# Kernel tuning notes

Measured on AMD Instinct MI355X. Metric: run time of the kernel, lower is better.

Reference implementation:

```python
import jax, jax.numpy as jnp
import numpy as np

# Model dims (ViT-Base @ 384)
L, H, D, HD, M, P, IMG, B, NC, CH = 12, 12, 768, 64, 3072, 16, 384, 32, 1000, 3
NPATCH = (IMG // P) ** 2  # 576
SCALE = 1.0 / np.sqrt(HD)


def setup_inputs() -> dict:
    key = jax.random.key(0)
    ks = iter(jax.random.split(key, 16))
    def n(shape, s=0.02):
        return (jax.random.normal(next(ks), shape, jnp.float32) * s).astype(jnp.float32)
    return dict(
        x=jax.random.normal(next(ks), (B, CH, IMG, IMG), jnp.float32),
        conv_w=n((D, CH, P, P)), conv_b=jnp.zeros((D,), jnp.float32),
        cls_token=jnp.zeros((1, 1, D), jnp.float32),
        pos_emb=n((1, NPATCH + 1, D), 1.0),
        ln1_g=jnp.ones((L, D), jnp.float32), ln1_b=jnp.zeros((L, D), jnp.float32),
        wqkv=n((L, H, D, 3 * HD)), bqkv=jnp.zeros((L, H, 3 * HD), jnp.float32),
        wmsa=n((L, D, D)), bmsa=jnp.zeros((L, D), jnp.float32),
        ln2_g=jnp.ones((L, D), jnp.float32), ln2_b=jnp.zeros((L, D), jnp.float32),
        lnm_g=jnp.ones((L, D), jnp.float32), lnm_b=jnp.zeros((L, D), jnp.float32),
        w1=n((L, D, M)), b1=jnp.zeros((L, M), jnp.float32),
        w2=n((L, M, D)), b2=jnp.zeros((L, D), jnp.float32),
        lnf_g=jnp.ones((D,), jnp.float32), lnf_b=jnp.zeros((D,), jnp.float32),
        whead=n((D, NC)), bhead=jnp.zeros((NC,), jnp.float32),
    )


def _ln(x, g, b, eps=1e-5):
    mu = jnp.mean(x, axis=-1, keepdims=True)
    var = jnp.mean(jnp.square(x - mu), axis=-1, keepdims=True)
    return (x - mu) * jax.lax.rsqrt(var + eps) * g + b


def _encoder_block(x, p):
    (ln1_g, ln1_b, wqkv, bqkv, wmsa, bmsa,
     ln2_g, ln2_b, lnm_g, lnm_b, w1, b1, w2, b2) = p
    b = x.shape[0]
    h = _ln(x, ln1_g, ln1_b)
    # batched per-head QKV (math identical to looping over H small Linears)
    qkv = jnp.einsum('bsd,hde->bhse', h, wqkv) + bqkv[:, None, :]  # [B,H,S,3*HD]
    q, k, v = jnp.split(qkv, 3, axis=-1)
    attn = jax.nn.softmax(jnp.einsum('bhqe,bhke->bhqk', q, k) * SCALE, axis=-1)
    o = jnp.einsum('bhqk,bhke->bhqe', attn, v)          # [B,H,S,HD]
    o = o.transpose(0, 2, 1, 3).reshape(b, -1, D)        # concat heads along feature
    msa = jnp.einsum('bsd,de->bse', o, wmsa) + bmsa
    x1 = h + msa                                          # residual around MSA (post-LN1)
    h2 = _ln(x1, ln2_g, ln2_b)
    h2 = _ln(h2, lnm_g, lnm_b)                            # MLPBlock's own LayerNorm (double LN, faithful)
    mlp = jnp.einsum('bsm,md->bsd', jax.nn.gelu(jnp.einsum('bsd,dm->bsm', h2, w1) + b1, approximate=False), w2) + b2
    return x1 + mlp, None


def reference(x, conv_w, conv_b, cls_token, pos_emb,
              ln1_g, ln1_b, wqkv, bqkv, wmsa, bmsa,
              ln2_g, ln2_b, lnm_g, lnm_b, w1, b1, w2, b2,
              lnf_g, lnf_b, whead, bhead):
    b = x.shape[0]
    # patchify conv (image divisible by patch, so F.pad is a no-op)
    t = jax.lax.conv_general_dilated(x, conv_w, (P, P), 'VALID',
                                     dimension_numbers=('NCHW', 'OIHW', 'NCHW'))
    t = t + conv_b[None, :, None, None]
    # faithful to torch .view(b, -1, embed_dim) on NCHW layout (channel-major flatten)
    t = t.reshape(b, -1, D)
    n = t.shape[1]
    t = jnp.concatenate([jnp.broadcast_to(cls_token, (b, 1, D)), t], axis=1)
    t = t + pos_emb[:, :n + 1]
    stacked = (ln1_g, ln1_b, wqkv, bqkv, wmsa, bmsa,
               ln2_g, ln2_b, lnm_g, lnm_b, w1, b1, w2, b2)
    t, _ = jax.lax.scan(_encoder_block, t, stacked)
    y = _ln(t[:, 0], lnf_g, lnf_b)
    y = jax.nn.softmax(jnp.einsum('bd,dc->bc', y, whead) + bhead, axis=-1)
    return y
```

## Files before the change

### kernel.cpp

```cpp
#include <hip/hip_runtime.h>

using f16   = _Float16;
using f16x8 = __attribute__((ext_vector_type(8))) _Float16;
using f32x4 = __attribute__((ext_vector_type(4))) float;

#define MPAD  18560
#define MREAL 18464
#define MCONV 18432
#define SEQ   577
#define SPAD  640
#define NHEAD 12
#define NBATCH 32
#define SCALE_ 0.125f

__device__ __forceinline__ void load_lds16(const void* g, void* l) {
  __builtin_amdgcn_global_load_lds(
      (const __attribute__((address_space(1))) void*)g,
      (__attribute__((address_space(3))) void*)l, 16, 0, 0);
}

template<int K, int EPI>
__global__ __launch_bounds__(256) void gemm_k(
    const f16* __restrict__ A, const f16* __restrict__ Bt,
    const float* __restrict__ bias, const float* __restrict__ res,
    float* __restrict__ o32, f16* __restrict__ o16a, f16* __restrict__ o16b,
    f16* __restrict__ o16c, const float* __restrict__ pos,
    const float* __restrict__ lng, const float* __restrict__ lnb,
    const float* __restrict__ stats, int N, int Mreal)
{
  static_assert(K % 64 == 0, "BK=64");
  __shared__ __align__(16) f16 As[128 * 64];
  __shared__ __align__(16) f16 Bs[128 * 64];
  const int tid = threadIdx.x;
  const int lane = tid & 63, wv = tid >> 6;

  const int gx = gridDim.x, gy = gridDim.y;
  const int nwg = gx * gy;
  const int flat = blockIdx.y * gx + blockIdx.x;
  const int xcd = flat & 7;
  const int qq = nwg >> 3, rr = nwg & 7;
  const int p_ = ((xcd < rr) ? xcd * (qq + 1) : rr * (qq + 1) + (xcd - rr) * qq)
                 + (flat >> 3);
  const int bandsz = gy * 6;
  const int band = p_ / bandsz, within = p_ - band * bandsz;
  const int byi = within / 6;
  const int bxi = band * 6 + (within - byi * 6);
  const int bm = byi << 7, bn = bxi << 7;

  const int wm = (wv >> 1) << 6, wn = (wv & 1) << 6;
  const int r16 = lane & 15, g4 = lane >> 4;
  const f32x4 Z4 = {0.f, 0.f, 0.f, 0.f};

  f32x4 acc[4][4];
#pragma unroll
  for (int m = 0; m < 4; ++m)
#pragma unroll
    for (int n = 0; n < 4; ++n) acc[m][n] = Z4;

  const int srow = lane >> 3;
  const int sgc  = (lane & 7) ^ srow;
  const f16* Agp = A  + (size_t)(bm + srow) * K + sgc * 8;
  const f16* Bgp = Bt + (size_t)(bn + srow) * K + sgc * 8;

  for (int k0 = 0; k0 < K; k0 += 64) {
#pragma unroll
    for (int j = 0; j < 4; ++j) {
      const size_t roff = (size_t)((wv * 4 + j) * 8) * K + k0;
      load_lds16(Agp + roff, As + (wv * 4 + j) * 512);
      load_lds16(Bgp + roff, Bs + (wv * 4 + j) * 512);
    }
    __syncthreads();
#pragma unroll
    for (int ks = 0; ks < 2; ++ks) {
      f16x8 af[4], bf[4];
#pragma unroll
      for (int m = 0; m < 4; ++m) {
        int row = wm + m * 16 + r16;
        af[m] = *(const f16x8*)(As + row * 64 + ((((ks << 2) | g4) ^ (row & 7)) << 3));
      }
#pragma unroll
      for (int n = 0; n < 4; ++n) {
        int row = wn + n * 16 + r16;
        bf[n] = *(const f16x8*)(Bs + row * 64 + ((((ks << 2) | g4) ^ (row & 7)) << 3));
      }
#pragma unroll
      for (int m = 0; m < 4; ++m)
#pragma unroll
        for (int n = 0; n < 4; ++n)
          acc[m][n] = __builtin_amdgcn_mfma_f32_16x16x32_f16(af[m], bf[n], acc[m][n], 0, 0, 0);
    }
    __syncthreads();
  }

#pragma unroll
  for (int m = 0; m < 4; ++m) {
#pragma unroll
    for (int n = 0; n < 4; ++n) {
#pragma unroll
      for (int r = 0; r < 4; ++r) {
        int grow = bm + wm + m * 16 + g4 * 4 + r;
        int gcol = bn + wn + n * 16 + r16;
        float v = acc[m][n][r];
        if constexpr (EPI == 0) {
          if (grow < Mreal) {
            int b = grow / 576, p = grow - b * 576;
            int i = gcol * 576 + p;
            int sp = i / 768, dd = i - sp * 768;
            o32[((size_t)(b * SEQ + sp + 1)) * 768 + dd] =
                v + bias[gcol] + pos[(size_t)(sp + 1) * 768 + dd];
          }
        } else if constexpr (EPI == 1) {
          if (grow < Mreal) {
            int b = grow / SEQ, s = grow - b * SEQ;
            int hq = gcol / 192, rem = gcol - hq * 192;
            int sel = rem >> 6, e = rem & 63;
            float val = v + bias[gcol];
            int bh = b * NHEAD + hq;
            if (sel == 0)      o16a[((size_t)bh * SPAD + s) * 64 + e] = (f16)val;
            else if (sel == 1) o16b[((size_t)bh * SPAD + s) * 64 + e] = (f16)val;
            else               o16c[((size_t)bh * 64 + e) * SPAD + s] = (f16)val;
          }
        } else if constexpr (EPI == 2) {
          size_t idx = (size_t)grow * N + gcol;
          o32[idx] = v + bias[gcol] + res[idx];
        } else if constexpr (EPI == 4) {
          if (grow < Mreal) {
            size_t idx = (size_t)grow * N + gcol;
            float mu = stats[2 * grow], rs = stats[2 * grow + 1];
            float h = (res[idx] - mu) * rs * lng[gcol] + lnb[gcol];
            o32[idx] = v + bias[gcol] + h;
          }
        } else {
          float val = v + bias[gcol];
          float gl = 0.5f * val * (1.0f + erff(val * 0.70710678f));
          o16a[(size_t)grow * N + gcol] = (f16)gl;
        }
      }
    }
  }
}

__device__ __forceinline__ void block_red2(float& a, float& b, float* sm, int tid) {
  __syncthreads();
#pragma unroll
  for (int d = 32; d; d >>= 1) { a += __shfl_down(a, d); b += __shfl_down(b, d); }
  if ((tid & 63) == 0) { int w = tid >> 6; sm[w] = a; sm[w + 4] = b; }
  __syncthreads();
  a = sm[0] + sm[1] + sm[2] + sm[3];
  b = sm[4] + sm[5] + sm[6] + sm[7];
}

__global__ __launch_bounds__(256) void ln_fwd(const float* __restrict__ X,
    const float* __restrict__ g, const float* __restrict__ bb,
    float* __restrict__ stats, f16* __restrict__ hh)
{
  int row = blockIdx.x, tid = threadIdx.x;
  const float* x = X + (size_t)row * 768;
  float v0 = x[tid], v1 = x[tid + 256], v2 = x[tid + 512];
  float s = v0 + v1 + v2, s2 = v0*v0 + v1*v1 + v2*v2;
  __shared__ float sm[8];
  block_red2(s, s2, sm, tid);
  float mu = s * (1.f/768.f);
  float var = s2 * (1.f/768.f) - mu * mu;
  float rs = rsqrtf(var + 1e-5f);
  if (tid == 0) { stats[2 * row] = mu; stats[2 * row + 1] = rs; }
  size_t base = (size_t)row * 768;
  hh[base + tid      ] = (f16)((v0 - mu) * rs * g[tid      ] + bb[tid      ]);
  hh[base + tid + 256] = (f16)((v1 - mu) * rs * g[tid + 256] + bb[tid + 256]);
  hh[base + tid + 512] = (f16)((v2 - mu) * rs * g[tid + 512] + bb[tid + 512]);
}

__global__ __launch_bounds__(256) void ln2_fwd(const float* __restrict__ X,
    const float* __restrict__ g2, const float* __restrict__ bb2,
    const float* __restrict__ gm, const float* __restrict__ bbm,
    f16* __restrict__ hh)
{
  int row = blockIdx.x, tid = threadIdx.x;
  const float* x = X + (size_t)row * 768;
  float v0 = x[tid], v1 = x[tid + 256], v2 = x[tid + 512];
  float s = v0 + v1 + v2, s2 = v0*v0 + v1*v1 + v2*v2;
  __shared__ float sm[8];
  block_red2(s, s2, sm, tid);
  float mu = s * (1.f/768.f), var = s2 * (1.f/768.f) - mu * mu;
  float rs = rsqrtf(var + 1e-5f);
  float y0 = (v0 - mu) * rs * g2[tid      ] + bb2[tid      ];
  float y1 = (v1 - mu) * rs * g2[tid + 256] + bb2[tid + 256];
  float y2 = (v2 - mu) * rs * g2[tid + 512] + bb2[tid + 512];
  s = y0 + y1 + y2; s2 = y0*y0 + y1*y1 + y2*y2;
  block_red2(s, s2, sm, tid);
  mu = s * (1.f/768.f); var = s2 * (1.f/768.f) - mu * mu;
  rs = rsqrtf(var + 1e-5f);
  size_t base = (size_t)row * 768;
  hh[base + tid      ] = (f16)((y0 - mu) * rs * gm[tid      ] + bbm[tid      ]);
  hh[base + tid + 256] = (f16)((y1 - mu) * rs * gm[tid + 256] + bbm[tid + 256]);
  hh[base + tid + 512] = (f16)((y2 - mu) * rs * gm[tid + 512] + bbm[tid + 512]);
}

__global__ __launch_bounds__(256) void attn_k(const f16* __restrict__ qbuf,
    const f16* __restrict__ kbuf, const f16* __restrict__ vtbuf,
    f16* __restrict__ obuf)
{
  const int bh = blockIdx.y;
  const int b = bh / NHEAD, hd = bh - b * NHEAD;
  const int s0 = blockIdx.x << 6;
  const int tid = threadIdx.x, lane = tid & 63, wv = tid >> 6;
  const int r16 = lane & 15, g4 = lane >> 4;
  const f16* Q  = qbuf  + (size_t)bh * SPAD * 64;
  const f16* Kg = kbuf  + (size_t)bh * SPAD * 64;
  const f16* Vg = vtbuf + (size_t)bh * 64 * SPAD;
  __shared__ __align__(16) f16 Kt[64 * 64];
  __shared__ __align__(16) f16 Vt[64 * 64];
  __shared__ __align__(16) f16 Pw[4][16][72];
  const f32x4 Z4 = {0.f, 0.f, 0.f, 0.f};

  f16x8 qf[2];
  {
    const f16* qr = Q + (size_t)(s0 + wv * 16 + r16) * 64;
    qf[0] = *(const f16x8*)(qr + g4 * 8);
    qf[1] = *(const f16x8*)(qr + 32 + g4 * 8);
  }
  float m_run[4] = {-1e30f, -1e30f, -1e30f, -1e30f};
  float l_run[4] = {0.f, 0.f, 0.f, 0.f};
  f32x4 o_acc[4];
#pragma unroll
  for (int n = 0; n < 4; ++n) o_acc[n] = Z4;

  for (int kt = 0; kt < SPAD; kt += 64) {
#pragma unroll
    for (int j = 0; j < 2; ++j) {
      int off = (wv * 2 + j) * 1024 + lane * 16;
      int row = off >> 7;
      int cs  = (off >> 4) & 7;
      int gc  = cs ^ (row & 7);
      load_lds16(Kg + (size_t)(kt + row) * 64 + gc * 8, (void*)((char*)Kt + (wv*2 + j) * 1024));
      load_lds16(Vg + (size_t)row * SPAD + kt + gc * 8, (void*)((char*)Vt + (wv*2 + j) * 1024));
    }
    __syncthreads();

    f32x4 sa[4];
#pragma unroll
    for (int n = 0; n < 4; ++n) sa[n] = Z4;
#pragma unroll
    for (int n = 0; n < 4; ++n) {
      int krow = n * 16 + r16;
#pragma unroll
      for (int kc = 0; kc < 2; ++kc) {
        f16x8 kf = *(const f16x8*)(Kt + krow * 64 + (((kc * 4 + g4) ^ (krow & 7)) << 3));
        sa[n] = __builtin_amdgcn_mfma_f32_16x16x32_f16(qf[kc], kf, sa[n], 0, 0, 0);
      }
    }
#pragma unroll
    for (int r = 0; r < 4; ++r) {
      float mx = -1e30f;
#pragma unroll
      for (int n = 0; n < 4; ++n) {
        int key = kt + n * 16 + r16;
        float sv = (key < SEQ) ? sa[n][r] * SCALE_ : -1e30f;
        sa[n][r] = sv;
        mx = fmaxf(mx, sv);
      }
#pragma unroll
      for (int d = 1; d < 16; d <<= 1) mx = fmaxf(mx, __shfl_xor(mx, d));
      if (!__all(mx - m_run[r] <= 8.f)) {
        float mnew = fmaxf(m_run[r], mx);
        float alpha = __expf(m_run[r] - mnew);
        m_run[r] = mnew;
        l_run[r] *= alpha;
#pragma unroll
        for (int n = 0; n < 4; ++n) o_acc[n][r] *= alpha;
      }
      float ssum = 0.f;
#pragma unroll
      for (int n = 0; n < 4; ++n) {
        float p = __expf(sa[n][r] - m_run[r]);
        ssum += p;
        Pw[wv][g4 * 4 + r][n * 16 + r16] = (f16)p;
      }
#pragma unroll
      for (int d = 1; d < 16; d <<= 1) ssum += __shfl_xor(ssum, d);
      l_run[r] += ssum;
    }
    f16x8 pf[2];
    pf[0] = *(const f16x8*)(&Pw[wv][r16][g4 * 8]);
    pf[1] = *(const f16x8*)(&Pw[wv][r16][32 + g4 * 8]);
#pragma unroll
    for (int n = 0; n < 4; ++n) {
      int erow = n * 16 + r16;
#pragma unroll
      for (int kc = 0; kc < 2; ++kc) {
        f16x8 vf = *(const f16x8*)(Vt + erow * 64 + (((kc * 4 + g4) ^ (erow & 7)) << 3));
        o_acc[n] = __builtin_amdgcn_mfma_f32_16x16x32_f16(pf[kc], vf, o_acc[n], 0, 0, 0);
      }
    }
    __syncthreads();
  }
  float inv[4];
#pragma unroll
  for (int r = 0; r < 4; ++r) inv[r] = 1.f / l_run[r];
#pragma unroll
  for (int n = 0; n < 4; ++n)
#pragma unroll
    for (int r = 0; r < 4; ++r) {
      int s = s0 + wv * 16 + g4 * 4 + r;
      if (s < SEQ)
        obuf[((size_t)(b * SEQ + s)) * 768 + hd * 64 + n * 16 + r16] =
            (f16)(o_acc[n][r] * inv[r]);
    }
}

__global__ __launch_bounds__(256) void cvt_transpose(const float* __restrict__ in,
    f16* __restrict__ out, int K, int N, size_t ls_in, size_t ls_out)
{
  in  += (size_t)blockIdx.z * ls_in;
  out += (size_t)blockIdx.z * ls_out;
  __shared__ float t[32][33];
  int n0 = blockIdx.x << 5, k0 = blockIdx.y << 5;
  int tx = threadIdx.x & 31, ty = threadIdx.x >> 5;
#pragma unroll
  for (int i = 0; i < 4; ++i) t[ty + 8*i][tx] = in[(size_t)(k0 + ty + 8*i) * N + n0 + tx];
  __syncthreads();
#pragma unroll
  for (int i = 0; i < 4; ++i) out[(size_t)(n0 + ty + 8*i) * K + k0 + tx] = (f16)t[tx][ty + 8*i];
}

__global__ __launch_bounds__(256) void cvt_qkvw(const float* __restrict__ in,
    f16* __restrict__ out, size_t ls_in, size_t ls_out)
{
  in  += (size_t)blockIdx.z * ls_in;
  out += (size_t)blockIdx.z * ls_out;
  __shared__ float t[32][33];
  int n0 = blockIdx.x << 5, k0 = blockIdx.y << 5;
  int tx = threadIdx.x & 31, ty = threadIdx.x >> 5;
  int hq = n0 / 192, r0 = n0 - hq * 192;
#pragma unroll
  for (int i = 0; i < 4; ++i)
    t[ty + 8*i][tx] = in[(size_t)hq * 147456 + (size_t)(k0 + ty + 8*i) * 192 + r0 + tx];
  __syncthreads();
#pragma unroll
  for (int i = 0; i < 4; ++i) out[(size_t)(n0 + ty + 8*i) * 768 + k0 + tx] = (f16)t[tx][ty + 8*i];
}

__global__ __launch_bounds__(256) void cvt_plain(const float* __restrict__ in,
    f16* __restrict__ out, int n)
{
  int i = blockIdx.x * 1024 + threadIdx.x;
#pragma unroll
  for (int j = 0; j < 4; ++j) { int idx = i + j * 256; if (idx < n) out[idx] = (f16)in[idx]; }
}

__global__ __launch_bounds__(256) void zero_vpad(f16* __restrict__ vtb) {
  int bh = blockIdx.x;
  for (int idx = threadIdx.x; idx < 64 * (SPAD - SEQ); idx += 256) {
    int e = idx / (SPAD - SEQ), s = SEQ + idx - e * (SPAD - SEQ);
    vtb[((size_t)bh * 64 + e) * SPAD + s] = (f16)0.f;
  }
}

__global__ __launch_bounds__(256) void im2col_k(const float* __restrict__ x, f16* __restrict__ out) {
  int row = blockIdx.x;
  int b = row / 576, p = row - b * 576;
  int py = p / 24, px = p - py * 24;
  int tid = threadIdx.x;
#pragma unroll
  for (int j = 0; j < 3; ++j) {
    int k = tid + j * 256;
    int c = k >> 8, rem = k & 255;
    int iy = rem >> 4, ix = rem & 15;
    out[(size_t)row * 768 + k] =
        (f16)x[(((size_t)(b * 3 + c)) * 384 + py * 16 + iy) * 384 + px * 16 + ix];
  }
}

__global__ __launch_bounds__(256) void cls_k(const float* __restrict__ ct,
    const float* __restrict__ pos, float* __restrict__ X)
{
  int b = blockIdx.x, tid = threadIdx.x;
#pragma unroll
  for (int j = 0; j < 3; ++j) {
    int d0 = tid + j * 256;
    X[((size_t)b * SEQ) * 768 + d0] = ct[d0] + pos[d0];
  }
}

__global__ __launch_bounds__(256) void head_logits(const float* __restrict__ X,
    const float* __restrict__ g, const float* __restrict__ bb,
    const float* __restrict__ W, const float* __restrict__ bhd,
    float* __restrict__ lg)
{
  int b = blockIdx.x, tid = threadIdx.x;
  const float* x = X + (size_t)(b * SEQ) * 768;
  float v0 = x[tid], v1 = x[tid + 256], v2 = x[tid + 512];
  float s = v0 + v1 + v2, s2 = v0*v0 + v1*v1 + v2*v2;
  __shared__ float sm[8];
  block_red2(s, s2, sm, tid);
  float mu = s * (1.f/768.f), var = s2 * (1.f/768.f) - mu * mu;
  float rs = rsqrtf(var + 1e-5f);
  __shared__ float y[768];
  y[tid      ] = (v0 - mu) * rs * g[tid      ] + bb[tid      ];
  y[tid + 256] = (v1 - mu) * rs * g[tid + 256] + bb[tid + 256];
  y[tid + 512] = (v2 - mu) * rs * g[tid + 512] + bb[tid + 512];
  __syncthreads();
  int c = blockIdx.y * 250 + tid;
  if (tid < 250) {
    float a0 = 0.f, a1 = 0.f, a2 = 0.f, a3 = 0.f;
#pragma unroll 4
    for (int d = 0; d < 768; d += 4) {
      a0 = fmaf(y[d    ], W[(size_t)(d    ) * 1000 + c], a0);
      a1 = fmaf(y[d + 1], W[(size_t)(d + 1) * 1000 + c], a1);
      a2 = fmaf(y[d + 2], W[(size_t)(d + 2) * 1000 + c], a2);
      a3 = fmaf(y[d + 3], W[(size_t)(d + 3) * 1000 + c], a3);
    }
    lg[(size_t)b * 1000 + c] = (a0 + a1) + (a2 + a3) + bhd[c];
  }
}

__global__ __launch_bounds__(256) void head_soft(const float* __restrict__ lg,
    float* __restrict__ out)
{
  int b = blockIdx.x, tid = threadIdx.x;
  __shared__ float sm[8];
  float v[4], mx = -1e30f;
#pragma unroll
  for (int j = 0; j < 4; ++j) {
    int c = tid + j * 256;
    v[j] = (c < 1000) ? lg[(size_t)b * 1000 + c] : -1e30f;
    mx = fmaxf(mx, v[j]);
  }
#pragma unroll
  for (int d = 32; d; d >>= 1) mx = fmaxf(mx, __shfl_down(mx, d));
  if ((tid & 63) == 0) sm[tid >> 6] = mx;
  __syncthreads();
  mx = fmaxf(fmaxf(sm[0], sm[1]), fmaxf(sm[2], sm[3]));
  float se = 0.f, ex[4];
#pragma unroll
  for (int j = 0; j < 4; ++j) {
    int c = tid + j * 256;
    ex[j] = (c < 1000) ? __expf(v[j] - mx) : 0.f;
    se += ex[j];
  }
  __syncthreads();
#pragma unroll
  for (int d = 32; d; d >>= 1) se += __shfl_down(se, d);
  if ((tid & 63) == 0) sm[tid >> 6] = se;
  __syncthreads();
  se = sm[0] + sm[1] + sm[2] + sm[3];
  float inv = 1.f / se;
#pragma unroll
  for (int j = 0; j < 4; ++j) {
    int c = tid + j * 256;
    if (c < 1000) out[(size_t)b * 1000 + c] = ex[j] * inv;
  }
}

extern "C" void kernel_launch(void* const* d_in, const int* in_sizes, int n_in,
                              void* d_out, int out_size, void* d_ws, size_t ws_size,
                              hipStream_t stream)
{
  (void)in_sizes; (void)n_in; (void)out_size;
  const float* x      = (const float*)d_in[0];
  const float* conv_w = (const float*)d_in[1];
  const float* conv_b = (const float*)d_in[2];
  const float* cls_t  = (const float*)d_in[3];
  const float* pos    = (const float*)d_in[4];
  const float* ln1_g  = (const float*)d_in[5];
  const float* ln1_b  = (const float*)d_in[6];
  const float* wqkv   = (const float*)d_in[7];
  const float* bqkv   = (const float*)d_in[8];
  const float* wmsa   = (const float*)d_in[9];
  const float* bmsa   = (const float*)d_in[10];
  const float* ln2_g  = (const float*)d_in[11];
  const float* ln2_b  = (const float*)d_in[12];
  const float* lnm_g  = (const float*)d_in[13];
  const float* lnm_b  = (const float*)d_in[14];
  const float* w1     = (const float*)d_in[15];
  const float* b1     = (const float*)d_in[16];
  const float* w2     = (const float*)d_in[17];
  const float* b2     = (const float*)d_in[18];
  const float* lnf_g  = (const float*)d_in[19];
  const float* lnf_b  = (const float*)d_in[20];
  const float* whead  = (const float*)d_in[21];
  const float* bhead  = (const float*)d_in[22];
  float* out = (float*)d_out;

  const size_t szQ  = (size_t)2304 * 768;
  const size_t szM  = (size_t)768 * 768;
  const size_t szW1 = (size_t)3072 * 768;
  const size_t szW2 = (size_t)768 * 3072;
  const size_t fixed_bytes =
      (size_t)MPAD * 768 * 4 + (size_t)MPAD * 8 + 32 * 1000 * 4 +
      (size_t)MPAD * 768 * 2 +
      (size_t)MPAD * 3072 * 2 + 3 * ((size_t)NBATCH * NHEAD * SPAD * 64 * 2) +
      (size_t)768 * 768 * 2  + 16 * 256 ;
  const bool hoist =
      ws_size >= fixed_bytes + 12 * (szQ + szM + szW1 + szW2) * 2 + 8 * 256;
  const int LW = hoist ? 12 : 1;

  char* wsp = (char*)d_ws;
  size_t off = 0;
  auto alloc = [&](size_t bytes) {
    char* p = wsp + off; off += (bytes + 255) & ~(size_t)255; return p;
  };
  float* X    = (float*)alloc((size_t)MPAD * 768 * 4);
  float* stats= (float*)alloc((size_t)MPAD * 8);
  float* lgbuf= (float*)alloc((size_t)32 * 1000 * 4);
  f16*   hh   = (f16*)  alloc((size_t)MPAD * 768 * 2);
  f16*   abuf = (f16*)  alloc((size_t)MPAD * 3072 * 2);
  f16*   qb   = (f16*)  alloc((size_t)NBATCH * NHEAD * SPAD * 64 * 2);
  f16*   kb   = (f16*)  alloc((size_t)NBATCH * NHEAD * SPAD * 64 * 2);
  f16*   vtb  = (f16*)  alloc((size_t)NBATCH * NHEAD * SPAD * 64 * 2);
  f16*   WcT  = (f16*)  alloc((size_t)768 * 768 * 2);
  f16*   WqkvT= (f16*)  alloc(LW * szQ  * 2);
  f16*   WmsaT= (f16*)  alloc(LW * szM  * 2);
  f16*   W1T  = (f16*)  alloc(LW * szW1 * 2);
  f16*   W2T  = (f16*)  alloc(LW * szW2 * 2);
  f16*   obuf   = abuf;
  f16*   patchA = abuf;
  f16*   h2h    = hh;
  if (ws_size < off) return;

  zero_vpad<<<dim3(NBATCH * NHEAD), 256, 0, stream>>>(vtb);
  cvt_plain<<<dim3((768 * 768 + 1023) / 1024), 256, 0, stream>>>(conv_w, WcT, 768 * 768);
  if (hoist) {
    cvt_qkvw<<<dim3(72, 24, 12), 256, 0, stream>>>(wqkv, WqkvT, (size_t)12*768*192, szQ);
    cvt_transpose<<<dim3(24, 24, 12), 256, 0, stream>>>(wmsa, WmsaT, 768, 768, szM, szM);
    cvt_transpose<<<dim3(96, 24, 12), 256, 0, stream>>>(w1, W1T, 768, 3072, szW1, szW1);
    cvt_transpose<<<dim3(24, 96, 12), 256, 0, stream>>>(w2, W2T, 3072, 768, szW2, szW2);
  }
  im2col_k<<<dim3(MCONV), 256, 0, stream>>>(x, patchA);
  gemm_k<768, 0><<<dim3(6, 144), 256, 0, stream>>>(
      patchA, WcT, conv_b, nullptr, X, nullptr, nullptr, nullptr, pos,
      nullptr, nullptr, nullptr, 768, MCONV);
  cls_k<<<dim3(NBATCH), 256, 0, stream>>>(cls_t, pos, X);

  for (int l = 0; l < 12; ++l) {
    f16* wq  = WqkvT + (hoist ? (size_t)l * szQ  : 0);
    f16* wms = WmsaT + (hoist ? (size_t)l * szM  : 0);
    f16* w1t = W1T   + (hoist ? (size_t)l * szW1 : 0);
    f16* w2t = W2T   + (hoist ? (size_t)l * szW2 : 0);
    if (!hoist) {
      cvt_qkvw<<<dim3(72, 24), 256, 0, stream>>>(
          wqkv + (size_t)l * 12 * 768 * 192, wq, 0, 0);
      cvt_transpose<<<dim3(24, 24), 256, 0, stream>>>(
          wmsa + (size_t)l * 768 * 768, wms, 768, 768, 0, 0);
      cvt_transpose<<<dim3(96, 24), 256, 0, stream>>>(
          w1 + (size_t)l * 768 * 3072, w1t, 768, 3072, 0, 0);
      cvt_transpose<<<dim3(24, 96), 256, 0, stream>>>(
          w2 + (size_t)l * 3072 * 768, w2t, 3072, 768, 0, 0);
    }

    ln_fwd<<<dim3(MREAL), 256, 0, stream>>>(X, ln1_g + l * 768, ln1_b + l * 768, stats, hh);
    gemm_k<768, 1><<<dim3(18, 145), 256, 0, stream>>>(
        hh, wq, bqkv + (size_t)l * 2304, nullptr, nullptr, qb, kb, vtb, nullptr,
        nullptr, nullptr, nullptr, 2304, MREAL);
    attn_k<<<dim3(10, NBATCH * NHEAD), 256, 0, stream>>>(qb, kb, vtb, obuf);
    gemm_k<768, 4><<<dim3(6, 145), 256, 0, stream>>>(
        obuf, wms, bmsa + l * 768, X, X, nullptr, nullptr, nullptr, nullptr,
        ln1_g + l * 768, ln1_b + l * 768, stats, 768, MREAL);
    ln2_fwd<<<dim3(MREAL), 256, 0, stream>>>(
        X, ln2_g + l * 768, ln2_b + l * 768, lnm_g + l * 768, lnm_b + l * 768, h2h);
    gemm_k<768, 3><<<dim3(24, 145), 256, 0, stream>>>(
        h2h, w1t, b1 + (size_t)l * 3072, nullptr, nullptr, abuf, nullptr, nullptr, nullptr,
        nullptr, nullptr, nullptr, 3072, MREAL);
    gemm_k<3072, 2><<<dim3(6, 145), 256, 0, stream>>>(
        abuf, w2t, b2 + l * 768, X, X, nullptr, nullptr, nullptr, nullptr,
        nullptr, nullptr, nullptr, 768, MREAL);
  }
  head_logits<<<dim3(NBATCH, 4), 256, 0, stream>>>(X, lnf_g, lnf_b, whead, bhead, lgbuf);
  head_soft<<<dim3(NBATCH), 256, 0, stream>>>(lgbuf, out);
}
```

Measured before the change: 8.203 ms.

## Streamline attention softmax with exp2, deferred row sums, peeled mask, XCD remap

Folds log2(e) into the softmax scale so exponentials use exp2, and rescales the lazy-rescale threshold to match. Per-lane partial row sums are kept and reduced across lanes once at the end instead of every tile. The key-padding mask is applied only in a peeled final tile. Workgroup indices are remapped so neighbouring query tiles of the same head land on the same XCD for cache locality. These cut per-tile ALU and shuffle work, with small numerical differences from deferred summation.

```diff
diff --git a/kernel.cpp b/kernel.cpp
--- a/kernel.cpp
+++ b/kernel.cpp
@@ -11,7 +11,8 @@
 #define SPAD  640
 #define NHEAD 12
 #define NBATCH 32
-#define SCALE_ 0.125f
+#define SC2   0.18033688f
+#define THR2  11.5416f
 
 __device__ __forceinline__ void load_lds16(const void* g, void* l) {
   __builtin_amdgcn_global_load_lds(
@@ -200,9 +201,17 @@
     const f16* __restrict__ kbuf, const f16* __restrict__ vtbuf,
     f16* __restrict__ obuf)
 {
-  const int bh = blockIdx.y;
+  const int gx = gridDim.x;
+  const int nwg = gx * gridDim.y;
+  const int flat = blockIdx.y * gx + blockIdx.x;
+  const int xcd = flat & 7;
+  const int qq = nwg >> 3, rr = nwg & 7;
+  const int pos_ = ((xcd < rr) ? xcd * (qq + 1) : rr * (qq + 1) + (xcd - rr) * qq)
+                   + (flat >> 3);
+  const int bh = pos_ / gx;
+  const int s0 = (pos_ - bh * gx) << 6;
+
   const int b = bh / NHEAD, hd = bh - b * NHEAD;
-  const int s0 = blockIdx.x << 6;
   const int tid = threadIdx.x, lane = tid & 63, wv = tid >> 6;
   const int r16 = lane & 15, g4 = lane >> 4;
   const f16* Q  = qbuf  + (size_t)bh * SPAD * 64;
@@ -220,12 +229,12 @@
     qf[1] = *(const f16x8*)(qr + 32 + g4 * 8);
   }
   float m_run[4] = {-1e30f, -1e30f, -1e30f, -1e30f};
-  float l_run[4] = {0.f, 0.f, 0.f, 0.f};
+  float l_part[4] = {0.f, 0.f, 0.f, 0.f};
   f32x4 o_acc[4];
 #pragma unroll
   for (int n = 0; n < 4; ++n) o_acc[n] = Z4;
 
-  for (int kt = 0; kt < SPAD; kt += 64) {
+  auto tile = [&](int kt, bool mask) {
 #pragma unroll
     for (int j = 0; j < 2; ++j) {
       int off = (wv * 2 + j) * 1024 + lane * 16;
@@ -254,31 +263,27 @@
       float mx = -1e30f;
 #pragma unroll
       for (int n = 0; n < 4; ++n) {
-        int key = kt + n * 16 + r16;
-        float sv = (key < SEQ) ? sa[n][r] * SCALE_ : -1e30f;
+        float sv = sa[n][r] * SC2;
+        if (mask && (kt + n * 16 + r16 >= SEQ)) sv = -1e30f;
         sa[n][r] = sv;
         mx = fmaxf(mx, sv);
       }
 #pragma unroll
       for (int d = 1; d < 16; d <<= 1) mx = fmaxf(mx, __shfl_xor(mx, d));
-      if (!__all(mx - m_run[r] <= 8.f)) {
+      if (!__all(mx - m_run[r] <= THR2)) {
         float mnew = fmaxf(m_run[r], mx);
-        float alpha = __expf(m_run[r] - mnew);
+        float alpha = exp2f(m_run[r] - mnew);
         m_run[r] = mnew;
-        l_run[r] *= alpha;
+        l_part[r] *= alpha;
 #pragma unroll
         for (int n = 0; n < 4; ++n) o_acc[n][r] *= alpha;
       }
-      float ssum = 0.f;
 #pragma unroll
       for (int n = 0; n < 4; ++n) {
-        float p = __expf(sa[n][r] - m_run[r]);
-        ssum += p;
+        float p = exp2f(sa[n][r] - m_run[r]);
+        l_part[r] += p;
         Pw[wv][g4 * 4 + r][n * 16 + r16] = (f16)p;
       }
-#pragma unroll
-      for (int d = 1; d < 16; d <<= 1) ssum += __shfl_xor(ssum, d);
-      l_run[r] += ssum;
     }
     f16x8 pf[2];
     pf[0] = *(const f16x8*)(&Pw[wv][r16][g4 * 8]);
@@ -293,10 +298,20 @@
       }
     }
     __syncthreads();
-  }
+  };
+
+#pragma unroll 1
+  for (int kt = 0; kt < 576; kt += 64) tile(kt, false);
+  tile(576, true);
+
   float inv[4];
 #pragma unroll
-  for (int r = 0; r < 4; ++r) inv[r] = 1.f / l_run[r];
+  for (int r = 0; r < 4; ++r) {
+    float l = l_part[r];
+#pragma unroll
+    for (int d = 1; d < 16; d <<= 1) l += __shfl_xor(l, d);
+    inv[r] = 1.f / l;
+  }
 #pragma unroll
   for (int n = 0; n < 4; ++n)
 #pragma unroll
```

Result: faster. 7.831 ms (median of 3 runs) (-4.5%).
